# Kernel tuning notes

Measured on AMD Instinct MI355X. Metric: run time of the kernel, lower is better.

Reference implementation:

```python
import jax, jax.numpy as jnp
import numpy as np

# Le-ADMM constants (ADMM_Net init values; V_div_mat / R_div_mat are
# precomputed buffers in the torch code using these, not the learned mus)
MU1_0, MU2_0, MU3_0 = 1e-6, 1e-5, 4e-5
TAU_0 = 1e-4
ITERS = 5
BATCH = 8
SENSOR = (540, 960)


def _pad_full(v, sh):
    # zero-pad sensor-size (..., H, W) to full (..., 2H, 2W), centered
    H, W = sh
    pads = [(0, 0)] * (v.ndim - 2) + [(H // 2, H - H // 2), (W // 2, W - W // 2)]
    return jnp.pad(v, pads)


def _crop(v, sh):
    H, W = sh
    return v[..., H // 2:H // 2 + H, W // 2:W // 2 + W]


def _fft2(v):
    return jnp.fft.fft2(jnp.fft.ifftshift(v, axes=(-2, -1)), axes=(-2, -1))


def _ifft2(V):
    return jnp.fft.fftshift(jnp.fft.ifft2(V, axes=(-2, -1)), axes=(-2, -1))


def _Hop(x, Hf):
    return jnp.real(_ifft2(Hf * _fft2(x)))


def _Hadj(x, Hf):
    return jnp.real(_ifft2(jnp.conj(Hf) * _fft2(x)))


def _Psi(x):
    # forward finite differences (circular), vertical and horizontal
    return jnp.roll(x, 1, axis=-2) - x, jnp.roll(x, 1, axis=-1) - x


def _PsiT(uv, uh):
    return (jnp.roll(uv, -1, axis=-2) - uv) + (jnp.roll(uh, -1, axis=-1) - uh)


def _soft_iso(uv, uh, thresh):
    # isotropic soft-threshold on the 2D gradient magnitude
    mag = jnp.sqrt(uv * uv + uh * uh)
    mult = jnp.maximum(mag - thresh, 0.0) / jnp.maximum(mag, 1e-12)
    return uv * mult, uh * mult


def setup_inputs() -> dict:
    key = jax.random.key(0)
    k1, k2 = jax.random.split(key)
    x = jax.random.uniform(k1, (BATCH,) + SENSOR, dtype=jnp.float32)
    h = jax.random.uniform(k2, SENSOR, dtype=jnp.float32)
    h = h / jnp.linalg.norm(h)  # normalized PSF
    ones = jnp.ones((ITERS,), jnp.float32)
    return {
        "x": x,
        "h": h,
        "mu1": ones * MU1_0,
        "mu2": ones * MU2_0,
        "mu3": ones * MU3_0,
        "tau": ones * TAU_0,
    }


def reference(x, h, mu1, mu2, mu3, tau):
    sh = h.shape  # sensor size (H, W)
    fullH, fullW = 2 * sh[0], 2 * sh[1]

    Hf = _fft2(_pad_full(h[None], sh))[0]  # (2H, 2W) complex
    CtC = _pad_full(jnp.ones((1,) + sh, x.dtype), sh)[0]
    V_div = 1.0 / (CtC + MU1_0)
    lap = jnp.zeros((fullH, fullW), x.dtype)
    lap = (lap.at[0, 0].set(4.0).at[0, 1].set(-1.0).at[1, 0].set(-1.0)
           .at[0, -1].set(-1.0).at[-1, 0].set(-1.0))
    PsiTPsi = jnp.abs(jnp.fft.fft2(lap))
    R_div = 1.0 / (MU1_0 * jnp.abs(Hf) ** 2 + MU2_0 * PsiTPsi + MU3_0)

    Cty = _pad_full(x, sh)  # (B, 2H, 2W)
    zfull = jnp.zeros((x.shape[0], fullH, fullW), x.dtype)

    out = zfull
    for i in range(ITERS):
        # forward() calls admm.restValues() every iteration, so all ADMM state
        # (X, U, V, W, alphas) is zero at the start of each iteration: each
        # iteration is one ADMM step from zero state; output keeps the last.
        X, a1, a2v, a2h, a3 = zfull, zfull, zfull, zfull, zfull
        pv, ph = _Psi(X)
        Uv, Uh = _soft_iso(pv + a2v / mu2[i], ph + a2h / mu2[i], tau[i] / mu2[i])
        V = V_div * (a1 + mu1[i] * _Hop(X, Hf) + Cty)
        W = jnp.maximum(a3 / mu3[i] + X, 0.0)
        r = ((mu3[i] * W - a3)
             + _PsiT(mu2[i] * Uv - a2v, mu2[i] * Uh - a2h)
             + _Hadj(mu1[i] * V - a1, Hf))
        out = jnp.real(_ifft2(R_div * _fft2(r)))
    return _crop(out, sh)
```

## Files before the change

### kernel.cpp

```cpp
#include <hip/hip_runtime.h>


#define PI2 6.2831853071795864f

__device__ __forceinline__ float2 cadd(float2 a, float2 b){ return make_float2(a.x+b.x, a.y+b.y); }
__device__ __forceinline__ float2 csub(float2 a, float2 b){ return make_float2(a.x-b.x, a.y-b.y); }
__device__ __forceinline__ float2 cmul(float2 a, float2 b){ return make_float2(a.x*b.x - a.y*b.y, a.x*b.y + a.y*b.x); }
__device__ __forceinline__ float4 pk(float2 a, float2 b){ return make_float4(a.x,a.y,b.x,b.y); }

__device__ __forceinline__ int IDX(int a){ return a + (a >> 4); }
#define IDXSZ(n) ((n) + ((n) >> 4))
__device__ __forceinline__ int IDXP(int a){ return a + ((a >> 5) << 1); }
#define IDXPSZ(n) ((n) + (((n) >> 5) << 1) + 4)

__device__ __forceinline__ void ldp(const float2* __restrict__ b, int pos,
                                    float2& v0, float2& v1){
    const float4 t = *(const float4*)&b[IDXP(2*pos)];
    v0 = make_float2(t.x,t.y); v1 = make_float2(t.z,t.w);
}
__device__ __forceinline__ void stp(float2* __restrict__ b, int pos,
                                    float2 v0, float2 v1){
    *(float4*)&b[IDXP(2*pos)] = pk(v0, v1);
}

template<int DIR>
__device__ __forceinline__ void dft3(float2 x0, float2 x1, float2 x2,
                                     float2& y0, float2& y1, float2& y2)
{
    constexpr float s3 = (float)DIR * 0.8660254037844386f;
    float2 t = cadd(x1, x2), u = csub(x1, x2);
    float2 m = make_float2(x0.x - 0.5f*t.x, x0.y - 0.5f*t.y);
    float2 iu = make_float2(-s3*u.y, s3*u.x);
    y0 = cadd(x0, t); y1 = cadd(m, iu); y2 = csub(m, iu);
}

template<int DIR>
__device__ __forceinline__ void dft4(float2 a0, float2 a1, float2 a2, float2 a3,
                                     float2& b0, float2& b1, float2& b2, float2& b3)
{
    float2 t0 = cadd(a0,a2), t1 = csub(a0,a2), t2 = cadd(a1,a3), t3 = csub(a1,a3);
    float2 j3 = make_float2(-(float)DIR*t3.y, (float)DIR*t3.x);
    b0 = cadd(t0,t2); b2 = csub(t0,t2); b1 = cadd(t1,j3); b3 = csub(t1,j3);
}

template<int DIR>
__device__ __forceinline__ void dft6(const float2 a[6], float2 b[6])
{
    float2 e0,e1,e2,o0,o1,o2;
    dft3<DIR>(a[0],a[2],a[4], e0,e1,e2);
    dft3<DIR>(a[1],a[3],a[5], o0,o1,o2);
    constexpr float s3 = (float)DIR * 0.8660254037844386f;
    float2 w1 = make_float2( 0.5f, s3);
    float2 w2 = make_float2(-0.5f, s3);
    float2 t1 = cmul(w1,o1), t2 = cmul(w2,o2);
    b[0]=cadd(e0,o0); b[3]=csub(e0,o0);
    b[1]=cadd(e1,t1); b[4]=csub(e1,t1);
    b[2]=cadd(e2,t2); b[5]=csub(e2,t2);
}

template<int DIR>
__device__ __forceinline__ void dft8(const float2 a[8], float2 b[8])
{
    float2 e0,e1,e2,e3,o0,o1,o2,o3;
    dft4<DIR>(a[0],a[2],a[4],a[6], e0,e1,e2,e3);
    dft4<DIR>(a[1],a[3],a[5],a[7], o0,o1,o2,o3);
    constexpr float c = 0.70710678118654752f;
    float2 w1 = make_float2( c, (float)DIR*c);
    float2 w3 = make_float2(-c, (float)DIR*c);
    float2 t1 = cmul(w1,o1);
    float2 t2 = make_float2(-(float)DIR*o2.y, (float)DIR*o2.x);
    float2 t3 = cmul(w3,o3);
    b[0]=cadd(e0,o0); b[4]=csub(e0,o0);
    b[1]=cadd(e1,t1); b[5]=csub(e1,t1);
    b[2]=cadd(e2,t2); b[6]=csub(e2,t2);
    b[3]=cadd(e3,t3); b[7]=csub(e3,t3);
}

template<int DIR>
__device__ __forceinline__ void dft5(const float2 a[5], float2 b[5])
{
    constexpr float C1 = 0.30901699437494742f, S1c = 0.9510565162951535f;
    constexpr float C2 = -0.8090169943749475f, S2c = 0.5877852522924731f;
    float2 t1 = cadd(a[1],a[4]), t2 = cadd(a[2],a[3]), d1 = csub(a[1],a[4]), d2 = csub(a[2],a[3]);
    float2 m1 = make_float2(a[0].x + C1*t1.x + C2*t2.x, a[0].y + C1*t1.y + C2*t2.y);
    float2 m2 = make_float2(a[0].x + C2*t1.x + C1*t2.x, a[0].y + C2*t1.y + C1*t2.y);
    float2 e1 = make_float2(S1c*d1.x + S2c*d2.x, S1c*d1.y + S2c*d2.y);
    float2 e2 = make_float2(S2c*d1.x - S1c*d2.x, S2c*d1.y - S1c*d2.y);
    float2 ie1 = make_float2(-(float)DIR*e1.y, (float)DIR*e1.x);
    float2 ie2 = make_float2(-(float)DIR*e2.y, (float)DIR*e2.x);
    b[0] = make_float2(a[0].x + t1.x + t2.x, a[0].y + t1.y + t2.y);
    b[1] = cadd(m1, ie1); b[4] = csub(m1, ie1);
    b[2] = cadd(m2, ie2); b[3] = csub(m2, ie2);
}

template<int DIR, int R, int NCUR, int S>
__device__ __forceinline__ void mid_stage(const float2* __restrict__ src,
                                          float2* __restrict__ dst, int tid)
{
    constexpr int M  = NCUR / R;
    constexpr int NB = M * S;
    constexpr float STEP = (float)DIR * PI2 / (float)NCUR;
    for (int i = tid; i < NB; i += 256) {
        const int p = i / S;
        float2 a[R], b[R];
        #pragma unroll
        for (int t = 0; t < R; ++t) a[t] = src[IDX(i + S*M*t)];
        if constexpr (R == 6) dft6<DIR>(a,b); else dft8<DIR>(a,b);
        float sv, cv; __sincosf(STEP * (float)p, &sv, &cv);
        float2 w1 = make_float2(cv, sv), w = w1;
        b[1] = cmul(b[1], w);
        #pragma unroll
        for (int u = 2; u < R; ++u) { w = cmul(w, w1); b[u] = cmul(b[u], w); }
        const int ob = (i - p*S) + S*(R*p);
        #pragma unroll
        for (int u = 0; u < R; ++u) dst[IDX(ob + S*u)] = b[u];
    }
}

template<int DIR, int NCUR, int SC>
__device__ __forceinline__ void mid_pair(const float2* __restrict__ src,
                                         float2* __restrict__ dst, int tid)
{
    constexpr int NB = 180;
    constexpr float STEP = (float)DIR * PI2 / (float)NCUR;
    for (int ic = tid; ic < NB; ic += 256) {
        const int p = ic / SC;
        float2 a0[6], a1[6], b0[6], b1[6];
        #pragma unroll
        for (int t = 0; t < 6; ++t) ldp(src, ic + NB*t, a0[t], a1[t]);
        dft6<DIR>(a0,b0); dft6<DIR>(a1,b1);
        float sv, cv; __sincosf(STEP*(float)p, &sv, &cv);
        float2 w1 = make_float2(cv,sv), w = w1;
        b0[1]=cmul(b0[1],w); b1[1]=cmul(b1[1],w);
        #pragma unroll
        for (int u = 2; u < 6; ++u){ w = cmul(w,w1); b0[u]=cmul(b0[u],w); b1[u]=cmul(b1[u],w); }
        const int ob = (ic - p*SC) + SC*6*p;
        #pragma unroll
        for (int u = 0; u < 6; ++u) stp(dst, ob + SC*u, b0[u], b1[u]);
    }
}

template<int DIR, int NCUR, int SC>
__device__ __forceinline__ void mid_pair_ip(float2* __restrict__ buf, int tid)
{
    constexpr int NB = 180;
    constexpr float STEP = (float)DIR * PI2 / (float)NCUR;
    const bool act = tid < NB;
    float2 b0[6], b1[6]; int ob = 0;
    if (act) {
        const int p = tid / SC;
        float2 a0[6], a1[6];
        #pragma unroll
        for (int t = 0; t < 6; ++t) ldp(buf, tid + NB*t, a0[t], a1[t]);
        dft6<DIR>(a0,b0); dft6<DIR>(a1,b1);
        float sv, cv; __sincosf(STEP*(float)p, &sv, &cv);
        float2 w1 = make_float2(cv,sv), w = w1;
        b0[1]=cmul(b0[1],w); b1[1]=cmul(b1[1],w);
        #pragma unroll
        for (int u = 2; u < 6; ++u){ w = cmul(w,w1); b0[u]=cmul(b0[u],w); b1[u]=cmul(b1[u],w); }
        ob = (tid - p*SC) + SC*6*p;
    }
    __syncthreads();
    if (act) {
        #pragma unroll
        for (int u = 0; u < 6; ++u) stp(buf, ob + SC*u, b0[u], b1[u]);
    }
    __syncthreads();
}

__device__ __forceinline__ void col_s1_fwd_pair(const float2* __restrict__ g, int c0,
                                                float2* __restrict__ bA, int tid)
{
    constexpr float STEP = -PI2 / 1080.0f;
    const float2 z = make_float2(0.f,0.f);
    const float4* gc = (const float4*)(g + c0);
    for (int p = tid; p < 180; p += 256) {
        float2 a0[6], a1[6], b0[6], b1[6];
        a0[0]=a0[5]=a1[0]=a1[5]=z;
        if (p >= 90) { float4 t = gc[(p-90)*960]; a0[1]=make_float2(t.x,t.y); a1[1]=make_float2(t.z,t.w); }
        else         { a0[1]=a1[1]=z; }
        { float4 t = gc[(p+90)*960];  a0[2]=make_float2(t.x,t.y); a1[2]=make_float2(t.z,t.w); }
        { float4 t = gc[(p+270)*960]; a0[3]=make_float2(t.x,t.y); a1[3]=make_float2(t.z,t.w); }
        if (p < 90)  { float4 t = gc[(p+450)*960]; a0[4]=make_float2(t.x,t.y); a1[4]=make_float2(t.z,t.w); }
        else         { a0[4]=a1[4]=z; }
        dft6<-1>(a0,b0); dft6<-1>(a1,b1);
        float sv, cv; __sincosf(STEP*(float)p, &sv, &cv);
        float2 w1 = make_float2(cv,sv), w = w1;
        b0[1]=cmul(b0[1],w); b1[1]=cmul(b1[1],w);
        #pragma unroll
        for (int u = 2; u < 6; ++u){ w = cmul(w,w1); b0[u]=cmul(b0[u],w); b1[u]=cmul(b1[u],w); }
        #pragma unroll
        for (int u = 0; u < 6; ++u) stp(bA, 6*p + u, b0[u], b1[u]);
    }
}

__device__ __forceinline__ void fused5K5_ip(float2* __restrict__ buf,
                                            const float4* __restrict__ KI,
                                            int cpair, int tid)
{
    constexpr float STEP = PI2 / 1080.0f;
    const float4* Kc = KI + cpair*1080;
    const bool act = tid < 216;
    float2 d0[5], d1[5];
    if (act) {
        float2 a0[5],a1[5],s0[5],s1[5];
        #pragma unroll
        for (int u = 0; u < 5; ++u) ldp(buf, tid + 216*u, a0[u], a1[u]);
        dft5<-1>(a0,s0); dft5<-1>(a1,s1);
        #pragma unroll
        for (int u = 0; u < 5; ++u) {
            float4 kk = Kc[tid + 216*u];
            s0[u] = cmul(s0[u], make_float2(kk.x,kk.y));
            s1[u] = cmul(s1[u], make_float2(kk.z,kk.w));
        }
        dft5<1>(s0,d0); dft5<1>(s1,d1);
        float sv, cv; __sincosf(STEP*(float)tid, &sv, &cv);
        float2 w1 = make_float2(cv,sv), w = w1;
        d0[1]=cmul(d0[1],w); d1[1]=cmul(d1[1],w);
        #pragma unroll
        for (int u = 2; u < 5; ++u){ w = cmul(w,w1); d0[u]=cmul(d0[u],w); d1[u]=cmul(d1[u],w); }
    }
    __syncthreads();
    if (act) {
        #pragma unroll
        for (int u = 0; u < 5; ++u) stp(buf, 5*tid + u, d0[u], d1[u]);
    }
    __syncthreads();
}

__device__ __forceinline__ void fin6_crop_pair(const float2* __restrict__ src,
                                               float2* __restrict__ Zp,
                                               int c0, int tid)
{
    float4* gc = (float4*)(Zp + c0);
    for (int m = tid; m < 180; m += 256) {
        float2 a0[6],a1[6],b0[6],b1[6];
        #pragma unroll
        for (int t = 0; t < 6; ++t) ldp(src, m + 180*t, a0[t], a1[t]);
        dft6<1>(a0,b0); dft6<1>(a1,b1);
        gc[(m+270)*960] = pk(b0[0], b1[0]);
        if (m < 90)  gc[(m+450)*960] = pk(b0[1], b1[1]);
        if (m >= 90) gc[(m-90)*960]  = pk(b0[4], b1[4]);
        gc[(m+90)*960]  = pk(b0[5], b1[5]);
    }
}


template<bool HASB>
__device__ __forceinline__ void row_s1_fwd(const float* __restrict__ xa,
                                           const float* __restrict__ xb,
                                           float2* __restrict__ bA, int tid)
{
    constexpr float STEP = -PI2 / 1920.0f;
    const float2 z = make_float2(0.f,0.f);
    for (int p = tid; p < 240; p += 256) {
        float2 a[8], b[8];
        a[0]=z; a[1]=z; a[6]=z; a[7]=z;
        a[2] = make_float2(xa[p],     HASB ? xb[p]     : 0.f);
        a[3] = make_float2(xa[p+240], HASB ? xb[p+240] : 0.f);
        a[4] = make_float2(xa[p+480], HASB ? xb[p+480] : 0.f);
        a[5] = make_float2(xa[p+720], HASB ? xb[p+720] : 0.f);
        dft8<-1>(a,b);
        float sv, cv; __sincosf(STEP * (float)p, &sv, &cv);
        float2 w1 = make_float2(cv, sv), w = w1;
        b[1] = cmul(b[1], w);
        #pragma unroll
        for (int u = 2; u < 8; ++u) { w = cmul(w, w1); b[u] = cmul(b[u], w); }
        #pragma unroll
        for (int u = 0; u < 8; ++u) bA[IDX(8*p + u)] = b[u];
    }
}

__device__ __forceinline__ void row_s1_inv(const float2* __restrict__ Zp,
                                           float2* __restrict__ bA, int tid)
{
    constexpr float STEP = PI2 / 1920.0f;
    for (int p = tid; p < 240; p += 256) {
        float2 a[8], b[8];
        #pragma unroll
        for (int t = 0; t < 8; ++t) a[t] = Zp[p + 240*t];
        dft8<1>(a,b);
        float sv, cv; __sincosf(STEP * (float)p, &sv, &cv);
        float2 w1 = make_float2(cv, sv), w = w1;
        b[1] = cmul(b[1], w);
        #pragma unroll
        for (int u = 2; u < 8; ++u) { w = cmul(w, w1); b[u] = cmul(b[u], w); }
        #pragma unroll
        for (int u = 0; u < 8; ++u) bA[IDX(8*p + u)] = b[u];
    }
}

template<int DIR>
__device__ __forceinline__ void row_fin5_store(const float2* __restrict__ src,
                                               float2* __restrict__ gdst, int tid)
{
    for (int q = tid; q < 384; q += 256) {
        float2 a[5], b[5];
        #pragma unroll
        for (int u = 0; u < 5; ++u) a[u] = src[IDX(q + 384*u)];
        dft5<DIR>(a,b);
        #pragma unroll
        for (int u = 0; u < 5; ++u) gdst[q + 384*u] = b[u];
    }
}


__global__ __launch_bounds__(256,5) void k_row_fft_h(const float* __restrict__ h,
                                                     float2* __restrict__ Hrow)
{
    __shared__ float2 bA[IDXSZ(1920)], bB[IDXSZ(1920)];
    const int tid = threadIdx.x, r = blockIdx.x;
    row_s1_fwd<false>(h + r*960, nullptr, bA, tid); __syncthreads();
    mid_stage<-1,8,240, 8>(bA, bB, tid); __syncthreads();
    mid_stage<-1,6, 30,64>(bB, bA, tid); __syncthreads();
    row_fin5_store<-1>(bA, Hrow + r*1920, tid);
}

__global__ __launch_bounds__(256,4) void k_col_fft_h_buildK(const float2* __restrict__ Hrow,
                                                            const float* __restrict__ mu1,
                                                            float4* __restrict__ KI)
{
    __shared__ float2 bA[IDXPSZ(2160)], bB[IDXPSZ(2160)];
    const int tid = threadIdx.x;
    const int xcd = blockIdx.x & 7, idx = blockIdx.x >> 3;
    const int cpair = xcd*120 + idx, c0 = cpair*2;
    col_s1_fwd_pair(Hrow, c0, bA, tid);  __syncthreads();
    mid_pair<-1,180, 6>(bA, bB, tid);    __syncthreads();
    mid_pair<-1, 30,36>(bB, bA, tid);    __syncthreads();
    const float sc = mu1[4] / ((1.0f + 1e-6f) * 2073600.0f);
    const float cos0 = __cosf(PI2 * (float)(c0  ) * (1.0f/1920.0f));
    const float cos1 = __cosf(PI2 * (float)(c0+1) * (1.0f/1920.0f));
    float4* Kc = KI + cpair*1080;
    for (int p = tid; p < 216; p += 256) {
        float2 a0[5],a1[5],b0[5],b1[5];
        #pragma unroll
        for (int u = 0; u < 5; ++u) ldp(bA, p + 216*u, a0[u], a1[u]);
        dft5<-1>(a0,b0); dft5<-1>(a1,b1);
        #pragma unroll
        for (int u = 0; u < 5; ++u) {
            const int k = p + 216*u;
            const float cosk = __cosf(PI2 * (float)k * (1.0f/1080.0f));
            float m0 = b0[u].x*b0[u].x + b0[u].y*b0[u].y;
            float m1 = b1[u].x*b1[u].x + b1[u].y*b1[u].y;
            float f0 = sc / (1e-6f*m0 + 1e-5f*(4.0f - 2.0f*cosk - 2.0f*cos0) + 4e-5f);
            float f1 = sc / (1e-6f*m1 + 1e-5f*(4.0f - 2.0f*cosk - 2.0f*cos1) + 4e-5f);
            Kc[k] = make_float4(f0*b0[u].x, -f0*b0[u].y, f1*b1[u].x, -f1*b1[u].y);
        }
    }
}

__global__ __launch_bounds__(256,5) void k_row_fft_x(const float* __restrict__ x,
                                                     float2* __restrict__ Z)
{
    __shared__ float2 bA[IDXSZ(1920)], bB[IDXSZ(1920)];
    const int tid = threadIdx.x;
    const int p = blockIdx.x / 540;
    const int r = blockIdx.x % 540;
    row_s1_fwd<true>(x + ((2*p)*540 + r)*960, x + ((2*p+1)*540 + r)*960, bA, tid);
    __syncthreads();
    mid_stage<-1,8,240, 8>(bA, bB, tid); __syncthreads();
    mid_stage<-1,6, 30,64>(bB, bA, tid); __syncthreads();
    row_fin5_store<-1>(bA, Z + (p*540 + r)*1920, tid);
}

__global__ __launch_bounds__(256,8) void k_col_fused(float2* __restrict__ Z,
                                                     const float4* __restrict__ KI)
{
    __shared__ float2 buf[IDXPSZ(2160)];
    const int tid = threadIdx.x;
    const int xcd = blockIdx.x & 7, idx = blockIdx.x >> 3;
    const int pp  = idx / 120;
    const int cpair = xcd*120 + (idx - pp*120), c0 = cpair*2;
    float2* Zp = Z + pp*540*1920;
    col_s1_fwd_pair(Zp, c0, buf, tid);  __syncthreads();
    mid_pair_ip<-1,180, 6>(buf, tid);
    mid_pair_ip<-1, 30,36>(buf, tid);
    fused5K5_ip(buf, KI, cpair, tid);
    mid_pair_ip< 1,216, 5>(buf, tid);
    mid_pair_ip< 1, 36,30>(buf, tid);
    fin6_crop_pair(buf, Zp, c0, tid);
}

__global__ __launch_bounds__(256,5) void k_row_ifft_out(const float2* __restrict__ Z,
                                                        float* __restrict__ out)
{
    __shared__ float2 bA[IDXSZ(1920)], bB[IDXSZ(1920)];
    const int tid = threadIdx.x;
    const int p = blockIdx.x / 540;
    const int r = blockIdx.x % 540;
    row_s1_inv(Z + (p*540 + r)*1920, bA, tid); __syncthreads();
    mid_stage<1,8,240, 8>(bA, bB, tid); __syncthreads();
    mid_stage<1,6, 30,64>(bB, bA, tid); __syncthreads();
    float* oa = out + ((2*p)*540 + r)*960;
    float* ob = out + ((2*p+1)*540 + r)*960;
    for (int q = tid; q < 384; q += 256) {
        float2 a[5], b[5];
        #pragma unroll
        for (int u = 0; u < 5; ++u) a[u] = bA[IDX(q + 384*u)];
        dft5<1>(a,b);
        oa[q+480] = b[0].x; ob[q+480] = b[0].y;
        if (q < 96)   { oa[q+864] = b[1].x; ob[q+864] = b[1].y; }
        if (q >= 288) { oa[q-288] = b[3].x; ob[q-288] = b[3].y; }
        oa[q+96]  = b[4].x; ob[q+96]  = b[4].y;
    }
}

extern "C" void kernel_launch(void* const* d_in, const int* in_sizes, int n_in,
                              void* d_out, int out_size, void* d_ws, size_t ws_size,
                              hipStream_t stream)
{
    (void)in_sizes; (void)n_in; (void)out_size; (void)ws_size;
    const float* x   = (const float*)d_in[0];
    const float* h   = (const float*)d_in[1];
    const float* mu1 = (const float*)d_in[2];
    float*       out = (float*)d_out;

    float4* KI   = (float4*)d_ws;
    float2* Z    = (float2*)d_ws + 2*960*1080;
    float2* Hrow = Z;

    k_row_fft_h       <<<540,    256, 0, stream>>>(h, Hrow);
    k_col_fft_h_buildK<<<960,    256, 0, stream>>>(Hrow, mu1, KI);
    k_row_fft_x       <<<4*540,  256, 0, stream>>>(x, Z);
    k_col_fused       <<<3840,   256, 0, stream>>>(Z, KI);
    k_row_ifft_out    <<<4*540,  256, 0, stream>>>(Z, out);
}
```

Measured before the change: 88.04 us.

## Process two rows per block in row FFTs and merge h/x row kernels

The row FFT kernels now handle two rows per block, using float4 shared storage and in-place radix stages, which halves the block count and puts more work in each thread. The h row FFT is folded into the same launch as the x row FFT, with Hrow moved to its own workspace region so the two no longer alias Z. This is meant to cut per-block overhead and barriers, and to remove one launch. It costs more registers per thread and introduces a dependency where the buildK kernel must wait on the merged kernel.

```diff
diff --git a/kernel.cpp b/kernel.cpp
--- a/kernel.cpp
+++ b/kernel.cpp
@@ -12,6 +12,8 @@
 #define IDXSZ(n) ((n) + ((n) >> 4))
 __device__ __forceinline__ int IDXP(int a){ return a + ((a >> 5) << 1); }
 #define IDXPSZ(n) ((n) + (((n) >> 5) << 1) + 4)
+__device__ __forceinline__ int IDX4(int a){ return a + (a >> 4); }
+#define IDX4SZ(n) ((n) + ((n) >> 4) + 2)
 
 __device__ __forceinline__ void ldp(const float2* __restrict__ b, int pos,
                                     float2& v0, float2& v1){
@@ -21,6 +23,15 @@
 __device__ __forceinline__ void stp(float2* __restrict__ b, int pos,
                                     float2 v0, float2 v1){
     *(float4*)&b[IDXP(2*pos)] = pk(v0, v1);
+}
+__device__ __forceinline__ void ld4(const float4* __restrict__ b, int pos,
+                                    float2& v0, float2& v1){
+    const float4 t = b[IDX4(pos)];
+    v0 = make_float2(t.x,t.y); v1 = make_float2(t.z,t.w);
+}
+__device__ __forceinline__ void st4(float4* __restrict__ b, int pos,
+                                    float2 v0, float2 v1){
+    b[IDX4(pos)] = pk(v0, v1);
 }
 
 template<int DIR>
@@ -93,6 +104,30 @@
     b[2] = cadd(m2, ie2); b[3] = csub(m2, ie2);
 }
 
+
+__device__ __forceinline__ void row_s1_fwd_h(const float* __restrict__ xa,
+                                             float2* __restrict__ bA, int tid)
+{
+    constexpr float STEP = -PI2 / 1920.0f;
+    const float2 z = make_float2(0.f,0.f);
+    for (int p = tid; p < 240; p += 256) {
+        float2 a[8], b[8];
+        a[0]=z; a[1]=z; a[6]=z; a[7]=z;
+        a[2] = make_float2(xa[p],     0.f);
+        a[3] = make_float2(xa[p+240], 0.f);
+        a[4] = make_float2(xa[p+480], 0.f);
+        a[5] = make_float2(xa[p+720], 0.f);
+        dft8<-1>(a,b);
+        float sv, cv; __sincosf(STEP * (float)p, &sv, &cv);
+        float2 w1 = make_float2(cv, sv), w = w1;
+        b[1] = cmul(b[1], w);
+        #pragma unroll
+        for (int u = 2; u < 8; ++u) { w = cmul(w, w1); b[u] = cmul(b[u], w); }
+        #pragma unroll
+        for (int u = 0; u < 8; ++u) bA[IDX(8*p + u)] = b[u];
+    }
+}
+
 template<int DIR, int R, int NCUR, int S>
 __device__ __forceinline__ void mid_stage(const float2* __restrict__ src,
                                           float2* __restrict__ dst, int tid)
@@ -117,56 +152,171 @@
     }
 }
 
-template<int DIR, int NCUR, int SC>
-__device__ __forceinline__ void mid_pair(const float2* __restrict__ src,
-                                         float2* __restrict__ dst, int tid)
-{
-    constexpr int NB = 180;
-    constexpr float STEP = (float)DIR * PI2 / (float)NCUR;
-    for (int ic = tid; ic < NB; ic += 256) {
-        const int p = ic / SC;
-        float2 a0[6], a1[6], b0[6], b1[6];
-        #pragma unroll
-        for (int t = 0; t < 6; ++t) ldp(src, ic + NB*t, a0[t], a1[t]);
-        dft6<DIR>(a0,b0); dft6<DIR>(a1,b1);
+__device__ __forceinline__ void row_fin5_store_h(const float2* __restrict__ src,
+                                                 float2* __restrict__ gdst, int tid)
+{
+    for (int q = tid; q < 384; q += 256) {
+        float2 a[5], b[5];
+        #pragma unroll
+        for (int u = 0; u < 5; ++u) a[u] = src[IDX(q + 384*u)];
+        dft5<-1>(a,b);
+        #pragma unroll
+        for (int u = 0; u < 5; ++u) gdst[q + 384*u] = b[u];
+    }
+}
+
+
+__device__ __forceinline__ void rp_s1_fwd(const float* __restrict__ xa,
+                                          const float* __restrict__ xb,
+                                          float4* __restrict__ sb, int tid)
+{
+    constexpr float STEP = -PI2 / 1920.0f;
+    const float2 z = make_float2(0.f,0.f);
+    for (int p = tid; p < 240; p += 256) {
+        float2 a0[8], a1[8], b0[8], b1[8];
+        a0[0]=a0[1]=a0[6]=a0[7]=z; a1[0]=a1[1]=a1[6]=a1[7]=z;
+        #pragma unroll
+        for (int t = 0; t < 4; ++t) {
+            a0[2+t] = make_float2(xa[p+240*t],     xb[p+240*t]);
+            a1[2+t] = make_float2(xa[960+p+240*t], xb[960+p+240*t]);
+        }
+        dft8<-1>(a0,b0); dft8<-1>(a1,b1);
         float sv, cv; __sincosf(STEP*(float)p, &sv, &cv);
         float2 w1 = make_float2(cv,sv), w = w1;
         b0[1]=cmul(b0[1],w); b1[1]=cmul(b1[1],w);
         #pragma unroll
-        for (int u = 2; u < 6; ++u){ w = cmul(w,w1); b0[u]=cmul(b0[u],w); b1[u]=cmul(b1[u],w); }
-        const int ob = (ic - p*SC) + SC*6*p;
-        #pragma unroll
-        for (int u = 0; u < 6; ++u) stp(dst, ob + SC*u, b0[u], b1[u]);
-    }
-}
-
-template<int DIR, int NCUR, int SC>
-__device__ __forceinline__ void mid_pair_ip(float2* __restrict__ buf, int tid)
-{
-    constexpr int NB = 180;
-    constexpr float STEP = (float)DIR * PI2 / (float)NCUR;
-    const bool act = tid < NB;
-    float2 b0[6], b1[6]; int ob = 0;
+        for (int u = 2; u < 8; ++u){ w = cmul(w,w1); b0[u]=cmul(b0[u],w); b1[u]=cmul(b1[u],w); }
+        #pragma unroll
+        for (int u = 0; u < 8; ++u) st4(sb, 8*p+u, b0[u], b1[u]);
+    }
+}
+
+__device__ __forceinline__ void rp_s1_inv(const float2* __restrict__ Zr0,
+                                          const float2* __restrict__ Zr1,
+                                          float4* __restrict__ sb, int tid)
+{
+    constexpr float STEP = PI2 / 1920.0f;
+    for (int p = tid; p < 240; p += 256) {
+        float2 a0[8], a1[8], b0[8], b1[8];
+        #pragma unroll
+        for (int t = 0; t < 8; ++t) { a0[t] = Zr0[p+240*t]; a1[t] = Zr1[p+240*t]; }
+        dft8<1>(a0,b0); dft8<1>(a1,b1);
+        float sv, cv; __sincosf(STEP*(float)p, &sv, &cv);
+        float2 w1 = make_float2(cv,sv), w = w1;
+        b0[1]=cmul(b0[1],w); b1[1]=cmul(b1[1],w);
+        #pragma unroll
+        for (int u = 2; u < 8; ++u){ w = cmul(w,w1); b0[u]=cmul(b0[u],w); b1[u]=cmul(b1[u],w); }
+        #pragma unroll
+        for (int u = 0; u < 8; ++u) st4(sb, 8*p+u, b0[u], b1[u]);
+    }
+}
+
+template<int DIR>
+__device__ __forceinline__ void rp_mid8_ip(float4* __restrict__ sb, int tid)
+{
+    constexpr float STEP = (float)DIR * PI2 / 240.0f;
+    const bool act = tid < 240;
+    float2 b0[8], b1[8]; int ob = 0;
     if (act) {
-        const int p = tid / SC;
+        const int p = tid >> 3;
+        float2 a0[8], a1[8];
+        #pragma unroll
+        for (int t = 0; t < 8; ++t) ld4(sb, tid + 240*t, a0[t], a1[t]);
+        dft8<DIR>(a0,b0); dft8<DIR>(a1,b1);
+        float sv, cv; __sincosf(STEP*(float)p, &sv, &cv);
+        float2 w1 = make_float2(cv,sv), w = w1;
+        b0[1]=cmul(b0[1],w); b1[1]=cmul(b1[1],w);
+        #pragma unroll
+        for (int u = 2; u < 8; ++u){ w = cmul(w,w1); b0[u]=cmul(b0[u],w); b1[u]=cmul(b1[u],w); }
+        ob = (tid - 8*p) + 64*p;
+    }
+    __syncthreads();
+    if (act) {
+        #pragma unroll
+        for (int u = 0; u < 8; ++u) st4(sb, ob + 8*u, b0[u], b1[u]);
+    }
+    __syncthreads();
+}
+
+template<int DIR>
+__device__ __forceinline__ void rp_mid6_ip(float4* __restrict__ sb, int tid)
+{
+    constexpr float STEP = (float)DIR * PI2 / 30.0f;
+    float2 c0[6], c1[6], d0[6], d1[6]; int ob0, ob1 = 0;
+    {
+        const int i = tid, p = i >> 6;
         float2 a0[6], a1[6];
         #pragma unroll
-        for (int t = 0; t < 6; ++t) ldp(buf, tid + NB*t, a0[t], a1[t]);
-        dft6<DIR>(a0,b0); dft6<DIR>(a1,b1);
-        float sv, cv; __sincosf(STEP*(float)p, &sv, &cv);
-        float2 w1 = make_float2(cv,sv), w = w1;
-        b0[1]=cmul(b0[1],w); b1[1]=cmul(b1[1],w);
-        #pragma unroll
-        for (int u = 2; u < 6; ++u){ w = cmul(w,w1); b0[u]=cmul(b0[u],w); b1[u]=cmul(b1[u],w); }
-        ob = (tid - p*SC) + SC*6*p;
-    }
-    __syncthreads();
-    if (act) {
-        #pragma unroll
-        for (int u = 0; u < 6; ++u) stp(buf, ob + SC*u, b0[u], b1[u]);
-    }
-    __syncthreads();
-}
+        for (int t = 0; t < 6; ++t) ld4(sb, i + 320*t, a0[t], a1[t]);
+        dft6<DIR>(a0,c0); dft6<DIR>(a1,c1);
+        float sv, cv; __sincosf(STEP*(float)p, &sv, &cv);
+        float2 w1 = make_float2(cv,sv), w = w1;
+        c0[1]=cmul(c0[1],w); c1[1]=cmul(c1[1],w);
+        #pragma unroll
+        for (int u = 2; u < 6; ++u){ w = cmul(w,w1); c0[u]=cmul(c0[u],w); c1[u]=cmul(c1[u],w); }
+        ob0 = (i - 64*p) + 384*p;
+    }
+    const bool act2 = tid < 64;
+    if (act2) {
+        const int i = 256 + tid;
+        float2 a0[6], a1[6];
+        #pragma unroll
+        for (int t = 0; t < 6; ++t) ld4(sb, i + 320*t, a0[t], a1[t]);
+        dft6<DIR>(a0,d0); dft6<DIR>(a1,d1);
+        float sv, cv; __sincosf(STEP*4.0f, &sv, &cv);
+        float2 w1 = make_float2(cv,sv), w = w1;
+        d0[1]=cmul(d0[1],w); d1[1]=cmul(d1[1],w);
+        #pragma unroll
+        for (int u = 2; u < 6; ++u){ w = cmul(w,w1); d0[u]=cmul(d0[u],w); d1[u]=cmul(d1[u],w); }
+        ob1 = tid + 1536;
+    }
+    __syncthreads();
+    {
+        #pragma unroll
+        for (int u = 0; u < 6; ++u) st4(sb, ob0 + 64*u, c0[u], c1[u]);
+    }
+    if (act2) {
+        #pragma unroll
+        for (int u = 0; u < 6; ++u) st4(sb, ob1 + 64*u, d0[u], d1[u]);
+    }
+    __syncthreads();
+}
+
+__device__ __forceinline__ void rp_fin5_storeZ(const float4* __restrict__ sb,
+                                               float2* __restrict__ Zr0,
+                                               float2* __restrict__ Zr1, int tid)
+{
+    for (int q = tid; q < 384; q += 256) {
+        float2 a0[5],a1[5],b0[5],b1[5];
+        #pragma unroll
+        for (int u = 0; u < 5; ++u) ld4(sb, q + 384*u, a0[u], a1[u]);
+        dft5<-1>(a0,b0); dft5<-1>(a1,b1);
+        #pragma unroll
+        for (int u = 0; u < 5; ++u) { Zr0[q+384*u] = b0[u]; Zr1[q+384*u] = b1[u]; }
+    }
+}
+
+__device__ __forceinline__ void rp_fin5_crop(const float4* __restrict__ sb,
+                                             float* __restrict__ oa0, float* __restrict__ ob0,
+                                             float* __restrict__ oa1, float* __restrict__ ob1,
+                                             int tid)
+{
+    for (int q = tid; q < 384; q += 256) {
+        float2 a0[5],a1[5],b0[5],b1[5];
+        #pragma unroll
+        for (int u = 0; u < 5; ++u) ld4(sb, q + 384*u, a0[u], a1[u]);
+        dft5<1>(a0,b0); dft5<1>(a1,b1);
+        oa0[q+480] = b0[0].x; ob0[q+480] = b0[0].y;
+        oa1[q+480] = b1[0].x; ob1[q+480] = b1[0].y;
+        if (q < 96)   { oa0[q+864] = b0[1].x; ob0[q+864] = b0[1].y;
+                        oa1[q+864] = b1[1].x; ob1[q+864] = b1[1].y; }
+        if (q >= 288) { oa0[q-288] = b0[3].x; ob0[q-288] = b0[3].y;
+                        oa1[q-288] = b1[3].x; ob1[q-288] = b1[3].y; }
+        oa0[q+96]  = b0[4].x; ob0[q+96]  = b0[4].y;
+        oa1[q+96]  = b1[4].x; ob1[q+96]  = b1[4].y;
+    }
+}
+
 
 __device__ __forceinline__ void col_s1_fwd_pair(const float2* __restrict__ g, int c0,
                                                 float2* __restrict__ bA, int tid)
@@ -194,6 +344,57 @@
     }
 }
 
+template<int DIR, int NCUR, int SC>
+__device__ __forceinline__ void mid_pair(const float2* __restrict__ src,
+                                         float2* __restrict__ dst, int tid)
+{
+    constexpr int NB = 180;
+    constexpr float STEP = (float)DIR * PI2 / (float)NCUR;
+    for (int ic = tid; ic < NB; ic += 256) {
+        const int p = ic / SC;
+        float2 a0[6], a1[6], b0[6], b1[6];
+        #pragma unroll
+        for (int t = 0; t < 6; ++t) ldp(src, ic + NB*t, a0[t], a1[t]);
+        dft6<DIR>(a0,b0); dft6<DIR>(a1,b1);
+        float sv, cv; __sincosf(STEP*(float)p, &sv, &cv);
+        float2 w1 = make_float2(cv,sv), w = w1;
+        b0[1]=cmul(b0[1],w); b1[1]=cmul(b1[1],w);
+        #pragma unroll
+        for (int u = 2; u < 6; ++u){ w = cmul(w,w1); b0[u]=cmul(b0[u],w); b1[u]=cmul(b1[u],w); }
+        const int ob = (ic - p*SC) + SC*6*p;
+        #pragma unroll
+        for (int u = 0; u < 6; ++u) stp(dst, ob + SC*u, b0[u], b1[u]);
+    }
+}
+
+template<int DIR, int NCUR, int SC>
+__device__ __forceinline__ void mid_pair_ip(float2* __restrict__ buf, int tid)
+{
+    constexpr int NB = 180;
+    constexpr float STEP = (float)DIR * PI2 / (float)NCUR;
+    const bool act = tid < NB;
+    float2 b0[6], b1[6]; int ob = 0;
+    if (act) {
+        const int p = tid / SC;
+        float2 a0[6], a1[6];
+        #pragma unroll
+        for (int t = 0; t < 6; ++t) ldp(buf, tid + NB*t, a0[t], a1[t]);
+        dft6<DIR>(a0,b0); dft6<DIR>(a1,b1);
+        float sv, cv; __sincosf(STEP*(float)p, &sv, &cv);
+        float2 w1 = make_float2(cv,sv), w = w1;
+        b0[1]=cmul(b0[1],w); b1[1]=cmul(b1[1],w);
+        #pragma unroll
+        for (int u = 2; u < 6; ++u){ w = cmul(w,w1); b0[u]=cmul(b0[u],w); b1[u]=cmul(b1[u],w); }
+        ob = (tid - p*SC) + SC*6*p;
+    }
+    __syncthreads();
+    if (act) {
+        #pragma unroll
+        for (int u = 0; u < 6; ++u) stp(buf, ob + SC*u, b0[u], b1[u]);
+    }
+    __syncthreads();
+}
+
 __device__ __forceinline__ void fused5K5_ip(float2* __restrict__ buf,
                                             const float4* __restrict__ KI,
                                             int cpair, int tid)
@@ -246,74 +447,32 @@
 }
 
 
-template<bool HASB>
-__device__ __forceinline__ void row_s1_fwd(const float* __restrict__ xa,
-                                           const float* __restrict__ xb,
-                                           float2* __restrict__ bA, int tid)
-{
-    constexpr float STEP = -PI2 / 1920.0f;
-    const float2 z = make_float2(0.f,0.f);
-    for (int p = tid; p < 240; p += 256) {
-        float2 a[8], b[8];
-        a[0]=z; a[1]=z; a[6]=z; a[7]=z;
-        a[2] = make_float2(xa[p],     HASB ? xb[p]     : 0.f);
-        a[3] = make_float2(xa[p+240], HASB ? xb[p+240] : 0.f);
-        a[4] = make_float2(xa[p+480], HASB ? xb[p+480] : 0.f);
-        a[5] = make_float2(xa[p+720], HASB ? xb[p+720] : 0.f);
-        dft8<-1>(a,b);
-        float sv, cv; __sincosf(STEP * (float)p, &sv, &cv);
-        float2 w1 = make_float2(cv, sv), w = w1;
-        b[1] = cmul(b[1], w);
-        #pragma unroll
-        for (int u = 2; u < 8; ++u) { w = cmul(w, w1); b[u] = cmul(b[u], w); }
-        #pragma unroll
-        for (int u = 0; u < 8; ++u) bA[IDX(8*p + u)] = b[u];
-    }
-}
-
-__device__ __forceinline__ void row_s1_inv(const float2* __restrict__ Zp,
-                                           float2* __restrict__ bA, int tid)
-{
-    constexpr float STEP = PI2 / 1920.0f;
-    for (int p = tid; p < 240; p += 256) {
-        float2 a[8], b[8];
-        #pragma unroll
-        for (int t = 0; t < 8; ++t) a[t] = Zp[p + 240*t];
-        dft8<1>(a,b);
-        float sv, cv; __sincosf(STEP * (float)p, &sv, &cv);
-        float2 w1 = make_float2(cv, sv), w = w1;
-        b[1] = cmul(b[1], w);
-        #pragma unroll
-        for (int u = 2; u < 8; ++u) { w = cmul(w, w1); b[u] = cmul(b[u], w); }
-        #pragma unroll
-        for (int u = 0; u < 8; ++u) bA[IDX(8*p + u)] = b[u];
-    }
-}
-
-template<int DIR>
-__device__ __forceinline__ void row_fin5_store(const float2* __restrict__ src,
-                                               float2* __restrict__ gdst, int tid)
-{
-    for (int q = tid; q < 384; q += 256) {
-        float2 a[5], b[5];
-        #pragma unroll
-        for (int u = 0; u < 5; ++u) a[u] = src[IDX(q + 384*u)];
-        dft5<DIR>(a,b);
-        #pragma unroll
-        for (int u = 0; u < 5; ++u) gdst[q + 384*u] = b[u];
-    }
-}
-
-
-__global__ __launch_bounds__(256,5) void k_row_fft_h(const float* __restrict__ h,
-                                                     float2* __restrict__ Hrow)
-{
-    __shared__ float2 bA[IDXSZ(1920)], bB[IDXSZ(1920)];
-    const int tid = threadIdx.x, r = blockIdx.x;
-    row_s1_fwd<false>(h + r*960, nullptr, bA, tid); __syncthreads();
-    mid_stage<-1,8,240, 8>(bA, bB, tid); __syncthreads();
-    mid_stage<-1,6, 30,64>(bB, bA, tid); __syncthreads();
-    row_fin5_store<-1>(bA, Hrow + r*1920, tid);
+__global__ __launch_bounds__(256,5) void k_row_fwd(const float* __restrict__ x,
+                                                   const float* __restrict__ h,
+                                                   float2* __restrict__ Z,
+                                                   float2* __restrict__ Hrow)
+{
+    __shared__ float4 sb[IDX4SZ(1920)];
+    const int tid = threadIdx.x;
+    if (blockIdx.x < 1080) {
+        const int pp = blockIdx.x / 270;
+        const int r0 = (blockIdx.x % 270) * 2;
+        const float* xa = x + ((2*pp  )*540 + r0)*960;
+        const float* xb = x + ((2*pp+1)*540 + r0)*960;
+        rp_s1_fwd(xa, xb, sb, tid); __syncthreads();
+        rp_mid8_ip<-1>(sb, tid);
+        rp_mid6_ip<-1>(sb, tid);
+        float2* Zr0 = Z + (pp*540 + r0)*1920;
+        rp_fin5_storeZ(sb, Zr0, Zr0 + 1920, tid);
+    } else {
+        float2* bA = (float2*)sb;
+        float2* bB = bA + IDXSZ(1920);
+        const int r = blockIdx.x - 1080;
+        row_s1_fwd_h(h + r*960, bA, tid); __syncthreads();
+        mid_stage<-1,8,240, 8>(bA, bB, tid); __syncthreads();
+        mid_stage<-1,6, 30,64>(bB, bA, tid); __syncthreads();
+        row_fin5_store_h(bA, Hrow + r*1920, tid);
+    }
 }
 
 __global__ __launch_bounds__(256,4) void k_col_fft_h_buildK(const float2* __restrict__ Hrow,
@@ -349,20 +508,6 @@
     }
 }
 
-__global__ __launch_bounds__(256,5) void k_row_fft_x(const float* __restrict__ x,
-                                                     float2* __restrict__ Z)
-{
-    __shared__ float2 bA[IDXSZ(1920)], bB[IDXSZ(1920)];
-    const int tid = threadIdx.x;
-    const int p = blockIdx.x / 540;
-    const int r = blockIdx.x % 540;
-    row_s1_fwd<true>(x + ((2*p)*540 + r)*960, x + ((2*p+1)*540 + r)*960, bA, tid);
-    __syncthreads();
-    mid_stage<-1,8,240, 8>(bA, bB, tid); __syncthreads();
-    mid_stage<-1,6, 30,64>(bB, bA, tid); __syncthreads();
-    row_fin5_store<-1>(bA, Z + (p*540 + r)*1920, tid);
-}
-
 __global__ __launch_bounds__(256,8) void k_col_fused(float2* __restrict__ Z,
                                                      const float4* __restrict__ KI)
 {
@@ -381,28 +526,20 @@
     fin6_crop_pair(buf, Zp, c0, tid);
 }
 
-__global__ __launch_bounds__(256,5) void k_row_ifft_out(const float2* __restrict__ Z,
-                                                        float* __restrict__ out)
-{
-    __shared__ float2 bA[IDXSZ(1920)], bB[IDXSZ(1920)];
+__global__ __launch_bounds__(256,5) void k_row_inv_out(const float2* __restrict__ Z,
+                                                       float* __restrict__ out)
+{
+    __shared__ float4 sb[IDX4SZ(1920)];
     const int tid = threadIdx.x;
-    const int p = blockIdx.x / 540;
-    const int r = blockIdx.x % 540;
-    row_s1_inv(Z + (p*540 + r)*1920, bA, tid); __syncthreads();
-    mid_stage<1,8,240, 8>(bA, bB, tid); __syncthreads();
-    mid_stage<1,6, 30,64>(bB, bA, tid); __syncthreads();
-    float* oa = out + ((2*p)*540 + r)*960;
-    float* ob = out + ((2*p+1)*540 + r)*960;
-    for (int q = tid; q < 384; q += 256) {
-        float2 a[5], b[5];
-        #pragma unroll
-        for (int u = 0; u < 5; ++u) a[u] = bA[IDX(q + 384*u)];
-        dft5<1>(a,b);
-        oa[q+480] = b[0].x; ob[q+480] = b[0].y;
-        if (q < 96)   { oa[q+864] = b[1].x; ob[q+864] = b[1].y; }
-        if (q >= 288) { oa[q-288] = b[3].x; ob[q-288] = b[3].y; }
-        oa[q+96]  = b[4].x; ob[q+96]  = b[4].y;
-    }
+    const int pp = blockIdx.x / 270;
+    const int r0 = (blockIdx.x % 270) * 2;
+    const float2* Zr0 = Z + (pp*540 + r0)*1920;
+    rp_s1_inv(Zr0, Zr0 + 1920, sb, tid); __syncthreads();
+    rp_mid8_ip<1>(sb, tid);
+    rp_mid6_ip<1>(sb, tid);
+    float* oa0 = out + ((2*pp  )*540 + r0)*960;
+    float* ob0 = out + ((2*pp+1)*540 + r0)*960;
+    rp_fin5_crop(sb, oa0, ob0, oa0 + 960, ob0 + 960, tid);
 }
 
 extern "C" void kernel_launch(void* const* d_in, const int* in_sizes, int n_in,
@@ -416,12 +553,11 @@
     float*       out = (float*)d_out;
 
     float4* KI   = (float4*)d_ws;
-    float2* Z    = (float2*)d_ws + 2*960*1080;
-    float2* Hrow = Z;
-
-    k_row_fft_h       <<<540,    256, 0, stream>>>(h, Hrow);
+    float2* Z    = (float2*)(KI + 960*1080);
+    float2* Hrow = Z + 4*540*1920;
+
+    k_row_fwd         <<<1620,   256, 0, stream>>>(x, h, Z, Hrow);
     k_col_fft_h_buildK<<<960,    256, 0, stream>>>(Hrow, mu1, KI);
-    k_row_fft_x       <<<4*540,  256, 0, stream>>>(x, Z);
     k_col_fused       <<<3840,   256, 0, stream>>>(Z, KI);
-    k_row_ifft_out    <<<4*540,  256, 0, stream>>>(Z, out);
-}
+    k_row_inv_out     <<<1080,   256, 0, stream>>>(Z, out);
+}
```

Result: faster. 84.37 us (-4.2%).
